# Performance work log

Hardware: AMD Instinct MI355X
Metric: run time of the kernel (lower is better)

## Reference

```python
import jax, jax.numpy as jnp
import numpy as np

N_NODES = 50000
N_EDGES = 600000
N_RELS = 19
D_IN = 128
D_HID = 64
D_OUT = 2


def setup_inputs() -> dict:
    key = jax.random.key(0)
    ks = jax.random.split(key, 10)
    feat = jax.random.normal(ks[0], (N_NODES, D_IN), dtype=jnp.float32)
    src = jax.random.randint(ks[1], (N_EDGES,), 0, N_NODES)
    dst = jax.random.randint(ks[2], (N_EDGES,), 0, N_NODES)
    etype = jax.random.randint(ks[3], (N_EDGES,), 0, N_RELS)
    s1 = 1.0 / np.sqrt(D_IN)
    s2 = 1.0 / np.sqrt(D_HID)
    W1 = jax.random.normal(ks[4], (N_RELS, D_IN, D_HID), dtype=jnp.float32) * s1
    loop1 = jax.random.normal(ks[5], (D_IN, D_HID), dtype=jnp.float32) * s1
    b1 = jnp.zeros((D_HID,), dtype=jnp.float32)
    W2 = jax.random.normal(ks[6], (N_RELS, D_HID, D_OUT), dtype=jnp.float32) * s2
    loop2 = jax.random.normal(ks[7], (D_HID, D_OUT), dtype=jnp.float32) * s2
    b2 = jnp.zeros((D_OUT,), dtype=jnp.float32)
    return {"feat": feat, "W1": W1, "loop1": loop1, "b1": b1,
            "W2": W2, "loop2": loop2, "b2": b2,
            "src": src, "dst": dst, "etype": etype}


def _rel_graph_conv(h, W, loop_w, bias, src, dst, etype, activation):
    # Per-relation transform of all nodes: [N, R, O]; then gather per edge.
    # (num_rels * out_feat is small, so this is cheaper than gathering W per edge.)
    transformed = jnp.einsum('nd,rdo->nro', h, W)
    msg = transformed[src, etype]                      # [E, O] edge messages
    agg = jax.ops.segment_sum(msg, dst, num_segments=h.shape[0])  # scatter-add
    out = agg + h @ loop_w + bias                      # self-loop + bias
    if activation is not None:
        out = activation(out)
    return out


def reference(feat, W1, loop1, b1, W2, loop2, b2, src, dst, etype):
    h = _rel_graph_conv(feat, W1, loop1, b1, src, dst, etype, jax.nn.relu)
    h = _rel_graph_conv(h, W2, loop2, b2, src, dst, etype, None)
    return h
```

## Files before the change

### kernel.cpp

```cpp
#include <hip/hip_runtime.h>

#define N_NODES 50000
#define N_EDGES 600000
#define N_RELS  19
#define D_IN    128
#define D_HID   64
#define D_OUT   2
#define EDGE_TILES ((N_EDGES + 127) / 128 + N_RELS)
#define SL_BLOCKS  ((N_NODES + 63) / 64)
#define PREP_BLOCKS ((N_RELS * D_HID * D_IN + N_RELS * 16 * D_HID + D_HID * D_IN + 255) / 256)

typedef unsigned short u16;
typedef unsigned int   u32;
typedef __attribute__((ext_vector_type(8))) short sfrag;
typedef __attribute__((ext_vector_type(4))) float f32x4;

__device__ __forceinline__ u16 f2bf(float f){
  union { float f; u32 i; } v; v.f = f;
  u32 r = v.i + 0x7fffu + ((v.i >> 16) & 1u);
  return (u16)(r >> 16);
}
__device__ __forceinline__ float bf2f(u16 u){
  union { u32 i; float f; } v; v.i = ((u32)u) << 16; return v.f;
}

__global__ __launch_bounds__(256) void k_fused_pre(const float* __restrict__ feat,
                                                   u16* __restrict__ featb,
                                                   const int* __restrict__ et,
                                                   const int* __restrict__ dst,
                                                   int* __restrict__ hist_rel,
                                                   int* __restrict__ hist_dst){
  int i = blockIdx.x * 256 + threadIdx.x;
  float2 f = ((const float2*)feat)[i];
  ((u32*)featb)[i] = (u32)f2bf(f.x) | ((u32)f2bf(f.y) << 16);
  if (blockIdx.x < (N_EDGES + 255) / 256) {
    __shared__ int lh[N_RELS];
    int tid = threadIdx.x;
    if (tid < N_RELS) lh[tid] = 0;
    __syncthreads();
    int e = blockIdx.x * 256 + tid;
    if (e < N_EDGES) {
      atomicAdd(&lh[et[e]], 1);
      atomicAdd(&hist_dst[dst[e]], 1);
    }
    __syncthreads();
    if (tid < N_RELS && lh[tid]) atomicAdd(&hist_rel[tid], lh[tid]);
  }
}

__global__ __launch_bounds__(256) void k_alloc_scan(
    const int* __restrict__ hist_dst, int* __restrict__ dstart,
    int* __restrict__ cur_dst, int* __restrict__ gcnt,
    const int* __restrict__ hist_rel, int* __restrict__ offs,
    int* __restrict__ toff, int* __restrict__ cur_rel,
    const float* __restrict__ W1, const float* __restrict__ loop1,
    const float* __restrict__ W2, u16* __restrict__ W1Tb,
    u16* __restrict__ loop1Tb, u16* __restrict__ W2Tb){
  if (blockIdx.x >= 197) {
    int idx = (blockIdx.x - 197) * 256 + threadIdx.x;
    const int T1 = N_RELS * D_HID * D_IN;
    const int T2 = T1 + N_RELS * 16 * D_HID;
    const int T3 = T2 + D_HID * D_IN;
    if (idx < T1) {
      int r = idx / (D_HID * D_IN);
      int t = idx - r * (D_HID * D_IN);
      int j = t >> 7, d = t & 127;
      W1Tb[idx] = f2bf(W1[(r * D_IN + d) * D_HID + j]);
    } else if (idx < T2) {
      int k2 = idx - T1;
      int r = k2 / (16 * D_HID);
      int t = k2 - r * (16 * D_HID);
      int n = t >> 6, k = t & 63;
      W2Tb[k2] = (n < D_OUT) ? f2bf(W2[(r * D_HID + k) * D_OUT + n]) : (u16)0;
    } else if (idx < T3) {
      int k2 = idx - T2;
      int j = k2 >> 7, d = k2 & 127;
      loop1Tb[k2] = f2bf(loop1[d * D_HID + j]);
    }
    return;
  }
  if (blockIdx.x == 196) {
    if (threadIdx.x == 0) {
      int acc = 0, tacc = 0;
      offs[0] = 0; toff[0] = 0;
      for (int r = 0; r < N_RELS; ++r) {
        cur_rel[r] = acc;
        int c = hist_rel[r];
        acc += c;                offs[r + 1] = acc;
        tacc += (c + 127) >> 7;  toff[r + 1] = tacc;
      }
    }
    return;
  }
  __shared__ int wbase[4];
  int tid = threadIdx.x, lane = tid & 63, wv = tid >> 6;
  int n = blockIdx.x * 256 + tid;
  int v = (n < N_NODES) ? hist_dst[n] : 0;
  int x = v;
  #pragma unroll
  for (int o = 1; o < 64; o <<= 1) { int u = __shfl_up(x, o); if (lane >= o) x += u; }
  if (lane == 63) wbase[wv] = atomicAdd(gcnt, x);
  __syncthreads();
  int start = wbase[wv] + x - v;
  if (n < N_NODES) { dstart[n] = start; cur_dst[n] = start; }
}

__global__ __launch_bounds__(256) void k_scatter_rel(const int* __restrict__ et,
                                                     int* __restrict__ cursor,
                                                     int* __restrict__ perm){
  __shared__ int lh[N_RELS], base[N_RELS];
  int tid = threadIdx.x;
  if (tid < N_RELS) lh[tid] = 0;
  __syncthreads();
  int e = blockIdx.x * 256 + tid;
  int r = 0, my = 0;
  bool valid = e < N_EDGES;
  if (valid) { r = et[e]; my = atomicAdd(&lh[r], 1); }
  __syncthreads();
  if (tid < N_RELS && lh[tid]) base[tid] = atomicAdd(&cursor[tid], lh[tid]);
  __syncthreads();
  if (valid) perm[base[r] + my] = e;
}

__global__ __launch_bounds__(256) void k_se1(
    const u16* __restrict__ featb, const u16* __restrict__ W1Tb,
    const u16* __restrict__ loop1Tb, const float* __restrict__ b1,
    const int* __restrict__ src, const int* __restrict__ dst,
    const int* __restrict__ perm, const int* __restrict__ offs,
    const int* __restrict__ toff, int* __restrict__ cur_dst,
    u16* __restrict__ msgbuf, float* __restrict__ agg1f){
  __shared__ __align__(16) u16 Als[128][136];
  __shared__ __align__(16) u16 Bls[64][136];
  __shared__ int posIds[128];
  int tid = threadIdx.x, lane = tid & 63, w = tid >> 6;
  int r16 = lane & 15, c4 = lane >> 4;

  if (blockIdx.x >= EDGE_TILES) {
    int base = (blockIdx.x - EDGE_TILES) * 64;
    { int j = tid >> 2, seg = tid & 3;
      const uint4* g = (const uint4*)(loop1Tb + j * 128) + seg * 4;
      uint4* d = (uint4*)&Bls[j][seg * 32];
      d[0] = g[0]; d[1] = g[1]; d[2] = g[2]; d[3] = g[3]; }
    { int i = tid >> 2, seg = tid & 3;
      int n = base + i; if (n >= N_NODES) n = N_NODES - 1;
      const uint4* g = (const uint4*)(featb + (size_t)n * D_IN) + seg * 4;
      uint4* d = (uint4*)&Als[i][seg * 32];
      d[0] = g[0]; d[1] = g[1]; d[2] = g[2]; d[3] = g[3]; }
    __syncthreads();
    sfrag aF[4];
    #pragma unroll
    for (int kk = 0; kk < 4; ++kk)
      aF[kk] = *(const sfrag*)&Als[w * 16 + r16][kk * 32 + c4 * 8];
    #pragma unroll
    for (int ct = 0; ct < 4; ++ct) {
      f32x4 acc = {0.f, 0.f, 0.f, 0.f};
      #pragma unroll
      for (int kk = 0; kk < 4; ++kk) {
        sfrag bF = *(const sfrag*)&Bls[ct * 16 + r16][kk * 32 + c4 * 8];
        acc = __builtin_amdgcn_mfma_f32_16x16x32_bf16(aF[kk], bF, acc, 0, 0, 0);
      }
      int col = ct * 16 + r16;
      float bias = b1[col];
      #pragma unroll
      for (int reg = 0; reg < 4; ++reg) {
        int row = base + w * 16 + c4 * 4 + reg;
        if (row < N_NODES) agg1f[(size_t)row * D_HID + col] = acc[reg] + bias;
      }
    }
    return;
  }

  int b = blockIdx.x;
  unsigned long long mm = __ballot((lane < N_RELS) && (b >= toff[lane + 1]));
  int rel = __popcll(mm);
  if (rel >= N_RELS) return;
  int ts = offs[rel] + ((b - toff[rel]) << 7);
  int vc = offs[rel + 1] - ts; if (vc > 128) vc = 128;

  {
    int j = tid >> 2, seg = tid & 3;
    const uint4* g = (const uint4*)(W1Tb + ((size_t)rel * 64 + j) * 128) + seg * 4;
    uint4* d = (uint4*)&Bls[j][seg * 32];
    d[0] = g[0]; d[1] = g[1]; d[2] = g[2]; d[3] = g[3];
  }
  #pragma unroll
  for (int p = 0; p < 2; ++p) {
    int i = p * 64 + (tid >> 2), seg = tid & 3;
    if (i < vc) {
      int e = perm[ts + i];
      if (seg == 0) posIds[i] = atomicAdd(&cur_dst[dst[e]], 1);
      const uint4* g = (const uint4*)(featb + (size_t)src[e] * D_IN) + seg * 4;
      uint4* d = (uint4*)&Als[i][seg * 32];
      d[0] = g[0]; d[1] = g[1]; d[2] = g[2]; d[3] = g[3];
    } else if (seg == 0) posIds[i] = -1;
  }
  __syncthreads();

  sfrag aF[2][4];
  #pragma unroll
  for (int mt = 0; mt < 2; ++mt)
    #pragma unroll
    for (int kk = 0; kk < 4; ++kk)
      aF[mt][kk] = *(const sfrag*)&Als[w * 32 + mt * 16 + r16][kk * 32 + c4 * 8];
  f32x4 accAll[2][4];
  #pragma unroll
  for (int ct = 0; ct < 4; ++ct) {
    sfrag bF[4];
    #pragma unroll
    for (int kk = 0; kk < 4; ++kk)
      bF[kk] = *(const sfrag*)&Bls[ct * 16 + r16][kk * 32 + c4 * 8];
    #pragma unroll
    for (int mt = 0; mt < 2; ++mt) {
      f32x4 acc = {0.f, 0.f, 0.f, 0.f};
      #pragma unroll
      for (int kk = 0; kk < 4; ++kk)
        acc = __builtin_amdgcn_mfma_f32_16x16x32_bf16(aF[mt][kk], bF[kk], acc, 0, 0, 0);
      accAll[mt][ct] = acc;
    }
  }
  float* msg = (float*)&Als[0][0];
  #pragma unroll
  for (int mt = 0; mt < 2; ++mt)
    #pragma unroll
    for (int ct = 0; ct < 4; ++ct) {
      int col = ct * 16 + r16;
      #pragma unroll
      for (int reg = 0; reg < 4; ++reg) {
        int row = w * 32 + mt * 16 + c4 * 4 + reg;
        msg[row * 68 + col] = accAll[mt][ct][reg];
      }
    }
  __syncthreads();
  { int row = tid >> 1, half = tid & 1;
    int pos = posIds[row];
    if (pos >= 0) {
      const float* mr = msg + row * 68 + half * 32;
      u32 pk[16];
      #pragma unroll
      for (int q = 0; q < 16; ++q)
        pk[q] = (u32)f2bf(mr[2 * q]) | ((u32)f2bf(mr[2 * q + 1]) << 16);
      uint4* d = (uint4*)(msgbuf + (size_t)pos * D_HID + half * 32);
      d[0] = *(uint4*)&pk[0];  d[1] = *(uint4*)&pk[4];
      d[2] = *(uint4*)&pk[8];  d[3] = *(uint4*)&pk[12];
    } }
}

__global__ __launch_bounds__(256) void k_agg_relu_self2(
    const u16* __restrict__ msgbuf, const int* __restrict__ dstart,
    const int* __restrict__ cnt, const float* __restrict__ agg1f,
    const float* __restrict__ loop2, const float* __restrict__ b2,
    u16* __restrict__ h1b, float* __restrict__ out){
  int wv = threadIdx.x >> 6, lane = threadIdx.x & 63;
  int n = blockIdx.x * 4 + wv;
  int s = dstart[n], epos = s + cnt[n];
  int h = lane >> 5, c = lane & 31;
  float a0 = 0.f, a1 = 0.f;
  for (int i = s + h; i < epos; i += 2) {
    u32 v = ((const u32*)msgbuf)[(size_t)i * 32 + c];
    a0 += bf2f((u16)(v & 0xffffu));
    a1 += bf2f((u16)(v >> 16));
  }
  a0 += __shfl_down(a0, 32);
  a1 += __shfl_down(a1, 32);
  float p0 = 0.f, p1 = 0.f;
  if (h == 0) {
    float2 sl = ((const float2*)(agg1f + (size_t)n * D_HID))[c];
    float v0 = a0 + sl.x, v1 = a1 + sl.y;
    v0 = v0 > 0.f ? v0 : 0.f;
    v1 = v1 > 0.f ? v1 : 0.f;
    ((u32*)h1b)[(size_t)n * 32 + c] = (u32)f2bf(v0) | ((u32)f2bf(v1) << 16);
    float2 w0 = ((const float2*)loop2)[2 * c];
    float2 w1 = ((const float2*)loop2)[2 * c + 1];
    p0 = v0 * w0.x + v1 * w1.x;
    p1 = v0 * w0.y + v1 * w1.y;
  }
  #pragma unroll
  for (int off = 16; off; off >>= 1) {
    p0 += __shfl_down(p0, off);
    p1 += __shfl_down(p1, off);
  }
  if (lane == 0) {
    out[n * 2]     = p0 + b2[0];
    out[n * 2 + 1] = p1 + b2[1];
  }
}

__global__ __launch_bounds__(256) void k_edge2_mfma(
    const u16* __restrict__ h1b, const u16* __restrict__ W2Tb,
    const int* __restrict__ src, const int* __restrict__ dst,
    const int* __restrict__ perm, const int* __restrict__ offs,
    const int* __restrict__ toff, float* __restrict__ out){
  __shared__ __align__(16) u16 Als[128][72];
  __shared__ __align__(16) u16 Bls[16][72];
  __shared__ int dstIds[128];
  int tid = threadIdx.x, lane = tid & 63, w = tid >> 6;

  int b = blockIdx.x;
  unsigned long long mm = __ballot((lane < N_RELS) && (b >= toff[lane + 1]));
  int rel = __popcll(mm);
  if (rel >= N_RELS) return;
  int ts = offs[rel] + ((b - toff[rel]) << 7);
  int vc = offs[rel + 1] - ts; if (vc > 128) vc = 128;

  if (tid < 128) {
    ((uint4*)&Bls[tid >> 3][0])[tid & 7] = ((const uint4*)(W2Tb + (size_t)rel * 16 * 64))[tid];
  }
  {
    int i = tid >> 1, half = tid & 1;
    if (i < vc) {
      int e = perm[ts + i];
      if (half == 0) dstIds[i] = dst[e];
      const uint4* g = (const uint4*)(h1b + (size_t)src[e] * D_HID) + half * 4;
      uint4* d = (uint4*)&Als[i][half * 32];
      d[0] = g[0]; d[1] = g[1]; d[2] = g[2]; d[3] = g[3];
    } else if (half == 0) dstIds[i] = -1;
  }
  __syncthreads();

  int r16 = lane & 15, c4 = lane >> 4;
  #pragma unroll
  for (int mt = 0; mt < 2; ++mt) {
    f32x4 acc = {0.f, 0.f, 0.f, 0.f};
    #pragma unroll
    for (int kk = 0; kk < 2; ++kk) {
      sfrag aF = *(const sfrag*)&Als[w * 32 + mt * 16 + r16][kk * 32 + c4 * 8];
      sfrag bF = *(const sfrag*)&Bls[r16][kk * 32 + c4 * 8];
      acc = __builtin_amdgcn_mfma_f32_16x16x32_bf16(aF, bF, acc, 0, 0, 0);
    }
    if (r16 < D_OUT) {
      #pragma unroll
      for (int reg = 0; reg < 4; ++reg) {
        int row = w * 32 + mt * 16 + c4 * 4 + reg;
        int dn = dstIds[row];
        if (dn >= 0) atomicAdd(&out[dn * D_OUT + r16], acc[reg]);
      }
    }
  }
}

extern "C" void kernel_launch(void* const* d_in, const int* in_sizes, int n_in,
                              void* d_out, int out_size, void* d_ws, size_t ws_size,
                              hipStream_t stream){
  const float* feat  = (const float*)d_in[0];
  const float* W1    = (const float*)d_in[1];
  const float* loop1 = (const float*)d_in[2];
  const float* b1    = (const float*)d_in[3];
  const float* W2    = (const float*)d_in[4];
  const float* loop2 = (const float*)d_in[5];
  const float* b2    = (const float*)d_in[6];
  const int* src     = (const int*)d_in[7];
  const int* dst     = (const int*)d_in[8];
  const int* et      = (const int*)d_in[9];
  float* out = (float*)d_out;

  char* w = (char*)d_ws;
  u16*   W1Tb     = (u16*)(w);
  u16*   W2Tb     = (u16*)(w + 311296);
  u16*   loop1Tb  = (u16*)(w + 350208);
  int*   hist_rel = (int*)(w + 366592);
  int*   gcnt     = (int*)(w + 366720);
  int*   hist_dst = (int*)(w + 366848);
  int*   offs     = (int*)(w + 566848);
  int*   toff     = (int*)(w + 566976);
  int*   cur_rel  = (int*)(w + 567104);
  int*   dstart   = (int*)(w + 567232);
  int*   cur_dst  = (int*)(w + 767232);
  int*   perm     = (int*)(w + 967232);
  u16*   featb    = (u16*)(w + 3367232);
  float* agg1f    = (float*)(w + 16167232);
  u16*   h1b      = (u16*)(w + 28967232);
  u16*   msgbuf   = (u16*)(w + 35367232);

  hipMemsetAsync(w + 366592, 0, 200256, stream);
  k_fused_pre     <<<12500, 256, 0, stream>>>(feat, featb, et, dst, hist_rel, hist_dst);
  k_alloc_scan    <<<197 + PREP_BLOCKS, 256, 0, stream>>>(
                      hist_dst, dstart, cur_dst, gcnt, hist_rel, offs, toff, cur_rel,
                      W1, loop1, W2, W1Tb, loop1Tb, W2Tb);
  k_scatter_rel   <<<2344,  256, 0, stream>>>(et, cur_rel, perm);
  k_se1           <<<EDGE_TILES + SL_BLOCKS, 256, 0, stream>>>(
                      featb, W1Tb, loop1Tb, b1, src, dst, perm, offs, toff,
                      cur_dst, msgbuf, agg1f);
  k_agg_relu_self2<<<12500, 256, 0, stream>>>(msgbuf, dstart, hist_dst, agg1f,
                                              loop2, b2, h1b, out);
  k_edge2_mfma    <<<EDGE_TILES, 256, 0, stream>>>(h1b, W2Tb, src, dst, perm, offs, toff, out);
}
```

Before: 317.6 us.

## Sort edges by relation and source-node bin to improve gather locality

Edges are now counting-sorted by (relation, src>>7) bucket instead of only by relation, so edge tiles in the first-layer and second-layer kernels gather source features from nearby rows. A per-bucket histogram is added to the preprocessing kernel and a block-wide prefix scan replaces the serial relation cursor. The scatter now does one global atomic per edge, which adds contention, and h1b is aliased onto the featb workspace to shrink the footprint. Relation boundaries are unchanged because buckets are ordered relation-major.

```diff
diff --git a/kernel.cpp b/kernel.cpp
--- a/kernel.cpp
+++ b/kernel.cpp
@@ -6,6 +6,8 @@
 #define D_IN    128
 #define D_HID   64
 #define D_OUT   2
+#define N_BINS  391
+#define N_BUCK  (N_RELS * N_BINS)
 #define EDGE_TILES ((N_EDGES + 127) / 128 + N_RELS)
 #define SL_BLOCKS  ((N_NODES + 63) / 64)
 #define PREP_BLOCKS ((N_RELS * D_HID * D_IN + N_RELS * 16 * D_HID + D_HID * D_IN + 255) / 256)
@@ -27,9 +29,11 @@
 __global__ __launch_bounds__(256) void k_fused_pre(const float* __restrict__ feat,
                                                    u16* __restrict__ featb,
                                                    const int* __restrict__ et,
+                                                   const int* __restrict__ src,
                                                    const int* __restrict__ dst,
                                                    int* __restrict__ hist_rel,
-                                                   int* __restrict__ hist_dst){
+                                                   int* __restrict__ hist_dst,
+                                                   int* __restrict__ hist_bk){
   int i = blockIdx.x * 256 + threadIdx.x;
   float2 f = ((const float2*)feat)[i];
   ((u32*)featb)[i] = (u32)f2bf(f.x) | ((u32)f2bf(f.y) << 16);
@@ -40,8 +44,10 @@
     __syncthreads();
     int e = blockIdx.x * 256 + tid;
     if (e < N_EDGES) {
-      atomicAdd(&lh[et[e]], 1);
+      int r = et[e];
+      atomicAdd(&lh[r], 1);
       atomicAdd(&hist_dst[dst[e]], 1);
+      atomicAdd(&hist_bk[r * N_BINS + (src[e] >> 7)], 1);
     }
     __syncthreads();
     if (tid < N_RELS && lh[tid]) atomicAdd(&hist_rel[tid], lh[tid]);
@@ -52,7 +58,8 @@
     const int* __restrict__ hist_dst, int* __restrict__ dstart,
     int* __restrict__ cur_dst, int* __restrict__ gcnt,
     const int* __restrict__ hist_rel, int* __restrict__ offs,
-    int* __restrict__ toff, int* __restrict__ cur_rel,
+    int* __restrict__ toff, const int* __restrict__ hist_bk,
+    int* __restrict__ cur_bk,
     const float* __restrict__ W1, const float* __restrict__ loop1,
     const float* __restrict__ W2, u16* __restrict__ W1Tb,
     u16* __restrict__ loop1Tb, u16* __restrict__ W2Tb){
@@ -80,11 +87,30 @@
     return;
   }
   if (blockIdx.x == 196) {
-    if (threadIdx.x == 0) {
+    __shared__ int wsum[4];
+    int tid = threadIdx.x, lane = tid & 63, wv = tid >> 6;
+    const int BPT = 30;
+    int base = tid * BPT;
+    int s = 0;
+    #pragma unroll
+    for (int q = 0; q < BPT; ++q) { int idx = base + q; if (idx < N_BUCK) s += hist_bk[idx]; }
+    int x = s;
+    #pragma unroll
+    for (int o = 1; o < 64; o <<= 1) { int u = __shfl_up(x, o); if (lane >= o) x += u; }
+    if (lane == 63) wsum[wv] = x;
+    __syncthreads();
+    int add = 0;
+    for (int j = 0; j < wv; ++j) add += wsum[j];
+    int run = x - s + add;
+    #pragma unroll
+    for (int q = 0; q < BPT; ++q) {
+      int idx = base + q;
+      if (idx < N_BUCK) { cur_bk[idx] = run; run += hist_bk[idx]; }
+    }
+    if (tid == 0) {
       int acc = 0, tacc = 0;
       offs[0] = 0; toff[0] = 0;
       for (int r = 0; r < N_RELS; ++r) {
-        cur_rel[r] = acc;
         int c = hist_rel[r];
         acc += c;                offs[r + 1] = acc;
         tacc += (c + 127) >> 7;  toff[r + 1] = tacc;
@@ -105,21 +131,16 @@
   if (n < N_NODES) { dstart[n] = start; cur_dst[n] = start; }
 }
 
-__global__ __launch_bounds__(256) void k_scatter_rel(const int* __restrict__ et,
-                                                     int* __restrict__ cursor,
+__global__ __launch_bounds__(256) void k_scatter_bin(const int* __restrict__ et,
+                                                     const int* __restrict__ src,
+                                                     int* __restrict__ cur_bk,
                                                      int* __restrict__ perm){
-  __shared__ int lh[N_RELS], base[N_RELS];
-  int tid = threadIdx.x;
-  if (tid < N_RELS) lh[tid] = 0;
-  __syncthreads();
-  int e = blockIdx.x * 256 + tid;
-  int r = 0, my = 0;
-  bool valid = e < N_EDGES;
-  if (valid) { r = et[e]; my = atomicAdd(&lh[r], 1); }
-  __syncthreads();
-  if (tid < N_RELS && lh[tid]) base[tid] = atomicAdd(&cursor[tid], lh[tid]);
-  __syncthreads();
-  if (valid) perm[base[r] + my] = e;
+  int e = blockIdx.x * 256 + threadIdx.x;
+  if (e < N_EDGES) {
+    int key = et[e] * N_BINS + (src[e] >> 7);
+    int pos = atomicAdd(&cur_bk[key], 1);
+    perm[pos] = e;
+  }
 }
 
 __global__ __launch_bounds__(256) void k_se1(
@@ -360,23 +381,25 @@
   int*   hist_rel = (int*)(w + 366592);
   int*   gcnt     = (int*)(w + 366720);
   int*   hist_dst = (int*)(w + 366848);
-  int*   offs     = (int*)(w + 566848);
-  int*   toff     = (int*)(w + 566976);
-  int*   cur_rel  = (int*)(w + 567104);
-  int*   dstart   = (int*)(w + 567232);
-  int*   cur_dst  = (int*)(w + 767232);
-  int*   perm     = (int*)(w + 967232);
-  u16*   featb    = (u16*)(w + 3367232);
-  float* agg1f    = (float*)(w + 16167232);
-  u16*   h1b      = (u16*)(w + 28967232);
-  u16*   msgbuf   = (u16*)(w + 35367232);
-
-  hipMemsetAsync(w + 366592, 0, 200256, stream);
-  k_fused_pre     <<<12500, 256, 0, stream>>>(feat, featb, et, dst, hist_rel, hist_dst);
+  int*   hist_bk  = (int*)(w + 566848);
+  int*   cur_bk   = (int*)(w + 596672);
+  int*   offs     = (int*)(w + 626496);
+  int*   toff     = (int*)(w + 626624);
+  int*   dstart   = (int*)(w + 626752);
+  int*   cur_dst  = (int*)(w + 826752);
+  int*   perm     = (int*)(w + 1026752);
+  u16*   featb    = (u16*)(w + 3426752);
+  u16*   h1b      = (u16*)(w + 3426752);
+  float* agg1f    = (float*)(w + 16226752);
+  u16*   msgbuf   = (u16*)(w + 29026752);
+
+  hipMemsetAsync(w + 366592, 0, 230080, stream);
+  k_fused_pre     <<<12500, 256, 0, stream>>>(feat, featb, et, src, dst,
+                                              hist_rel, hist_dst, hist_bk);
   k_alloc_scan    <<<197 + PREP_BLOCKS, 256, 0, stream>>>(
-                      hist_dst, dstart, cur_dst, gcnt, hist_rel, offs, toff, cur_rel,
-                      W1, loop1, W2, W1Tb, loop1Tb, W2Tb);
-  k_scatter_rel   <<<2344,  256, 0, stream>>>(et, cur_rel, perm);
+                      hist_dst, dstart, cur_dst, gcnt, hist_rel, offs, toff,
+                      hist_bk, cur_bk, W1, loop1, W2, W1Tb, loop1Tb, W2Tb);
+  k_scatter_bin   <<<2344,  256, 0, stream>>>(et, src, cur_bk, perm);
   k_se1           <<<EDGE_TILES + SL_BLOCKS, 256, 0, stream>>>(
                       featb, W1Tb, loop1Tb, b1, src, dst, perm, offs, toff,
                       cur_dst, msgbuf, agg1f);
```

Result: slower. 353.0 us (+11.2%).
